# Kernel tuning notes

Measured on AMD Instinct MI355X. Metric: run time of the kernel, lower is better.

Reference implementation:

```python
import jax, jax.numpy as jnp
import numpy as np

N = 40000   # nodes
E = 640000  # edges (before self-loops)
G = 64      # graphs
EPS = 1e-5


def _gat_conv(x, src, dst, W, a_src, a_dst, bias, n_nodes):
    """PyG GATConv, heads=1, leaky_relu slope 0.2, with self-loops already in src/dst."""
    h = x @ W.T                              # [N, out]
    s_score = h @ a_src                      # [N]
    d_score = h @ a_dst                      # [N]
    e = jax.nn.leaky_relu(s_score[src] + d_score[dst], 0.2)  # [E]
    m = jax.ops.segment_max(e, dst, num_segments=n_nodes)
    ex = jnp.exp(e - m[dst])
    z = jax.ops.segment_sum(ex, dst, num_segments=n_nodes)
    alpha = ex / z[dst]                      # per-dst softmax over incoming edges
    out = jax.ops.segment_sum(h[src] * alpha[:, None], dst, num_segments=n_nodes)
    return out + bias


def _layer_norm(x, gamma, beta):
    mu = jnp.mean(x, axis=-1, keepdims=True)
    var = jnp.mean((x - mu) ** 2, axis=-1, keepdims=True)
    return gamma * (x - mu) * jax.lax.rsqrt(var + EPS) + beta


def setup_inputs() -> dict:
    key = jax.random.key(0)
    ks = jax.random.split(key, 16)
    x = jax.random.normal(ks[0], (N, 128), dtype=jnp.float32)
    edge_index = jax.random.randint(ks[1], (2, E), 0, N, dtype=jnp.int32)
    batch = jnp.sort(jax.random.randint(ks[2], (N,), 0, G, dtype=jnp.int32))
    def glorot(k, shape):
        fan = shape[-1]
        return jax.random.normal(k, shape, dtype=jnp.float32) / jnp.sqrt(jnp.float32(fan))
    return {
        "x": x, "edge_index": edge_index, "batch": batch,
        "W1": glorot(ks[3], (128, 128)), "a1_src": glorot(ks[4], (128,)),
        "a1_dst": glorot(ks[5], (128,)), "b1": jnp.zeros((128,), jnp.float32),
        "g1": jnp.ones((128,), jnp.float32), "be1": jnp.zeros((128,), jnp.float32),
        "W2": glorot(ks[6], (64, 128)), "a2_src": glorot(ks[7], (64,)),
        "a2_dst": glorot(ks[8], (64,)), "b2": jnp.zeros((64,), jnp.float32),
        "g2": jnp.ones((64,), jnp.float32), "be2": jnp.zeros((64,), jnp.float32),
        "Wl": glorot(ks[9], (64, 64)), "bl": jnp.zeros((64,), jnp.float32),
        "Wc": glorot(ks[10], (1, 64)), "bc": jnp.zeros((1,), jnp.float32),
    }


def reference(x, edge_index, batch, W1, a1_src, a1_dst, b1, g1, be1,
              W2, a2_src, a2_dst, b2, g2, be2, Wl, bl, Wc, bc):
    # add self-loops as PyG GATConv does by default
    loops = jnp.arange(N, dtype=edge_index.dtype)
    src = jnp.concatenate([edge_index[0], loops])
    dst = jnp.concatenate([edge_index[1], loops])

    h = jax.nn.relu(_gat_conv(x, src, dst, W1, a1_src, a1_dst, b1, N))
    h = _layer_norm(h, g1, be1)
    h = jax.nn.relu(_gat_conv(h, src, dst, W2, a2_src, a2_dst, b2, N))
    h = _layer_norm(h, g2, be2)

    # global mean pool over graphs
    sums = jax.ops.segment_sum(h, batch, num_segments=G)          # [G, 64]
    cnt = jax.ops.segment_sum(jnp.ones((N,), h.dtype), batch, num_segments=G)
    pooled = sums / jnp.maximum(cnt, 1.0)[:, None]

    out = pooled @ Wl.T + bl
    out = out @ Wc.T + bc                                          # [G, 1]
    return out.squeeze(-1)                                         # [G]
```

## Files before the change

kernel.cpp:

```cpp
#include <hip/hip_runtime.h>
#include <hip/hip_fp16.h>
#include <math.h>

#define NNODES 40000
#define NEDGES 640000
#define NGRAPH 64
#define CAP 96
constexpr float LN_EPS = 1e-5f;


__device__ __forceinline__ float bf_sum(float v) {
    #pragma unroll
    for (int o = 32; o > 0; o >>= 1) v += __shfl_xor(v, o);
    return v;
}

__global__ void prep(const float* __restrict__ W1, const float* __restrict__ W2,
                     float* __restrict__ Wt1, float* __restrict__ Wt2,
                     int* __restrict__ cnt, float* __restrict__ sums) {
    int t = blockIdx.x * 256 + threadIdx.x;
    if (t < NNODES) cnt[t] = 0;
    if (t < 128 * 128) { int o = t / 128, i = t % 128; Wt1[i * 128 + o] = W1[t]; }
    if (t < 64 * 128)  { int o = t / 128, i = t % 128; Wt2[i * 64 + o] = W2[t]; }
    if (t < NGRAPH * 64) sums[t] = 0.f;
}

__global__ void bin_edges(const int* __restrict__ ei, int E,
                          int* __restrict__ cnt, unsigned short* __restrict__ ssrc) {
    int e = blockIdx.x * blockDim.x + threadIdx.x;
    if (e >= E) return;
    int s = ei[e], d = ei[E + e];
    int pos = atomicAdd(cnt + d, 1);
    if (pos < CAP) ssrc[d * CAP + pos] = (unsigned short)s;
}

template<int DIN, int DOUT, int NPT>
__global__ __launch_bounds__(256) void gemm_scores(
        const float* __restrict__ X, const float* __restrict__ Wt,
        const float* __restrict__ asrc, const float* __restrict__ adst,
        __half* __restrict__ H, float* __restrict__ S, float* __restrict__ Dv) {
    constexpr int CHG = DOUT / 4;
    constexpr int NG  = 256 / CHG;
    constexpr int NPB = NG * NPT;
    static_assert(NPB == 64, "NPB must be 64");
    __shared__ float xs[DIN][NPB];
    __shared__ float ps[NG][NPT][2];
    const int base = blockIdx.x * NPB;
    const int tid = threadIdx.x;
    #pragma unroll
    for (int i4 = tid; i4 < NPB * DIN / 4; i4 += 256) {
        const int nd = i4 % NPB, c4 = i4 / NPB;
        float4 v = *(const float4*)(X + (size_t)(base + nd) * DIN + 4 * c4);
        xs[4 * c4 + 0][nd] = v.x;
        xs[4 * c4 + 1][nd] = v.y;
        xs[4 * c4 + 2][nd] = v.z;
        xs[4 * c4 + 3][nd] = v.w;
    }
    __syncthreads();
    const int cg = tid % CHG, ng = tid / CHG;
    const int c0 = 4 * cg, n0 = ng * NPT;
    float acc[NPT][4];
    #pragma unroll
    for (int n = 0; n < NPT; ++n)
        #pragma unroll
        for (int k = 0; k < 4; ++k) acc[n][k] = 0.f;
    #pragma unroll 2
    for (int i = 0; i < DIN; ++i) {
        const float4 w = *(const float4*)(Wt + i * DOUT + c0);
        #pragma unroll
        for (int n4 = 0; n4 < NPT / 4; ++n4) {
            const float4 xv = *(const float4*)&xs[i][n0 + 4 * n4];
            const float xf[4] = {xv.x, xv.y, xv.z, xv.w};
            #pragma unroll
            for (int j = 0; j < 4; ++j) {
                const int n = 4 * n4 + j;
                acc[n][0] += xf[j] * w.x; acc[n][1] += xf[j] * w.y;
                acc[n][2] += xf[j] * w.z; acc[n][3] += xf[j] * w.w;
            }
        }
    }
    #pragma unroll
    for (int n = 0; n < NPT; ++n) {
        __half2 p01 = __floats2half2_rn(acc[n][0], acc[n][1]);
        __half2 p23 = __floats2half2_rn(acc[n][2], acc[n][3]);
        __half2* hp = (__half2*)(H + (size_t)(base + n0 + n) * DOUT + c0);
        hp[0] = p01; hp[1] = p23;
    }
    const float4 asf = *(const float4*)(asrc + c0);
    const float4 adf = *(const float4*)(adst + c0);
    float sp[NPT], dp[NPT];
    #pragma unroll
    for (int n = 0; n < NPT; ++n) {
        sp[n] = acc[n][0]*asf.x + acc[n][1]*asf.y + acc[n][2]*asf.z + acc[n][3]*asf.w;
        dp[n] = acc[n][0]*adf.x + acc[n][1]*adf.y + acc[n][2]*adf.z + acc[n][3]*adf.w;
    }
    #pragma unroll
    for (int o = CHG / 2; o > 0; o >>= 1) {
        #pragma unroll
        for (int n = 0; n < NPT; ++n) {
            sp[n] += __shfl_xor(sp[n], o);
            dp[n] += __shfl_xor(dp[n], o);
        }
    }
    if (cg == 0) {
        #pragma unroll
        for (int n = 0; n < NPT; ++n) { ps[ng][n][0] = sp[n]; ps[ng][n][1] = dp[n]; }
    }
    __syncthreads();
    if (tid < NPB) {
        S[base + tid]  = ps[tid / NPT][tid % NPT][0];
        Dv[base + tid] = ps[tid / NPT][tid % NPT][1];
    }
}

template<int D>
__device__ __forceinline__ void aggr_one_generic(
        const int node, const int deg, const int lane,
        const unsigned short* __restrict__ ssrc, const float* __restrict__ S,
        const float dsc, const __half* __restrict__ H,
        float& acc0, float& acc1, float& z) {
    constexpr int VPL = D / 64;
    float zz = 0.f;
    const int r0 = node * CAP;
    for (int bse = 0; bse < deg; bse += 64) {
        const int n = min(64, deg - bse);
        int s = 0; float a = 0.f;
        if (lane < n) {
            s = ssrc[r0 + bse + lane];
            float t = S[s] + dsc;
            t = t > 0.f ? t : 0.2f * t;
            a = __expf(t);
        }
        zz += bf_sum(a);
        const int abits = __float_as_int(a);
        for (int j = 0; j < n; ++j) {
            const int sj = __builtin_amdgcn_readlane(s, j);
            const float aj = __int_as_float(__builtin_amdgcn_readlane(abits, j));
            const __half* hp = H + (size_t)sj * D;
            if (VPL == 1) {
                acc0 += aj * __half2float(hp[lane]);
            } else {
                const float2 f = __half22float2(*(const __half2*)(hp + 2 * lane));
                acc0 += aj * f.x; acc1 += aj * f.y;
            }
        }
    }
    z = zz;
}

template<int D, int POOL>
__device__ __forceinline__ void finish_node(
        const int node, const int lane,
        float acc0, float acc1, float z, const float aself, const float2 selfF,
        const float* __restrict__ b, const float* __restrict__ gam,
        const float* __restrict__ bet,
        float* __restrict__ out, const int* __restrict__ batch,
        float* __restrict__ sums) {
    constexpr int VPL = D / 64;
    acc0 += aself * selfF.x;
    if (VPL == 2) acc1 += aself * selfF.y;
    z += aself;
    const float zinv = 1.0f / z;
    float vv[VPL], lsum = 0.f;
    vv[0] = acc0;
    if (VPL == 2) vv[1] = acc1;
    #pragma unroll
    for (int k = 0; k < VPL; ++k) {
        const int ch = VPL * lane + k;
        vv[k] = fmaxf(vv[k] * zinv + b[ch], 0.f);
        lsum += vv[k];
    }
    const float mu = bf_sum(lsum) / D;
    float q = 0.f;
    #pragma unroll
    for (int k = 0; k < VPL; ++k) { vv[k] -= mu; q += vv[k] * vv[k]; }
    const float rstd = rsqrtf(bf_sum(q) / D + LN_EPS);
    #pragma unroll
    for (int k = 0; k < VPL; ++k) {
        const int ch = VPL * lane + k;
        vv[k] = gam[ch] * vv[k] * rstd + bet[ch];
    }
    if (POOL) {
        const int bg = batch[node];
        atomicAdd(&sums[bg * D + lane], vv[0]);
    } else {
        if (VPL == 1) out[(size_t)node * D + lane] = vv[0];
        else *(float2*)(out + (size_t)node * D + 2 * lane) = make_float2(vv[0], vv[1]);
    }
}

template<int D, int POOL>
__global__ __launch_bounds__(256) void gat_aggr(
        const int* __restrict__ cnt, const unsigned short* __restrict__ ssrc,
        const float* __restrict__ S, const float* __restrict__ Dv,
        const __half* __restrict__ H,
        const float* __restrict__ b, const float* __restrict__ gam,
        const float* __restrict__ bet,
        float* __restrict__ out, const int* __restrict__ batch,
        float* __restrict__ sums) {
    constexpr int VPL = D / 64;
    const int lane = threadIdx.x & 63;
    const int wv   = threadIdx.x >> 6;
    const int nodeA = blockIdx.x * 8 + wv * 2;
    const int nodeB = nodeA + 1;

    const int degA = min(__builtin_amdgcn_readfirstlane(cnt[nodeA]), CAP);
    const int degB = min(__builtin_amdgcn_readfirstlane(cnt[nodeB]), CAP);
    const float dscA = Dv[nodeA], dscB = Dv[nodeB];

    float tsA = S[nodeA] + dscA; tsA = tsA > 0.f ? tsA : 0.2f * tsA;
    float tsB = S[nodeB] + dscB; tsB = tsB > 0.f ? tsB : 0.2f * tsB;
    const float aselfA = __expf(tsA);
    const float aselfB = __expf(tsB);

    float2 selfFA, selfFB;
    if (VPL == 1) {
        selfFA = make_float2(__half2float(H[(size_t)nodeA * D + lane]), 0.f);
        selfFB = make_float2(__half2float(H[(size_t)nodeB * D + lane]), 0.f);
    } else {
        selfFA = __half22float2(*(const __half2*)(H + (size_t)nodeA * D + 2 * lane));
        selfFB = __half22float2(*(const __half2*)(H + (size_t)nodeB * D + 2 * lane));
    }

    float accA0 = 0.f, accA1 = 0.f, accB0 = 0.f, accB1 = 0.f;
    float zA, zB;

    if (degA <= 64 && degB <= 64) {
        int sA = 0, sB = 0;
        if (lane < degA) sA = ssrc[nodeA * CAP + lane];
        if (lane < degB) sB = ssrc[nodeB * CAP + lane];
        float tA = S[sA] + dscA;
        float tB = S[sB] + dscB;
        tA = tA > 0.f ? tA : 0.2f * tA;
        tB = tB > 0.f ? tB : 0.2f * tB;
        const float aA = (lane < degA) ? __expf(tA) : 0.f;
        const float aB = (lane < degB) ? __expf(tB) : 0.f;
        zA = bf_sum(aA);
        zB = bf_sum(aB);
        const int abA = __float_as_int(aA), abB = __float_as_int(aB);

        const int nmA = (degA + 7) & ~7;
        const int nmB = (degB + 7) & ~7;
        const int nmax = max(nmA, nmB);
        for (int j = 0; j < nmax; j += 8) {
            const bool doA = j < nmA, doB = j < nmB;
            float afA[8], afB[8];
            __half2 hvA[8], hvB[8];
            __half hsA[8], hsB[8];
            if (doA) {
                #pragma unroll
                for (int u = 0; u < 8; ++u) {
                    const int sj = __builtin_amdgcn_readlane(sA, j + u);
                    afA[u] = __int_as_float(__builtin_amdgcn_readlane(abA, j + u));
                    const __half* hp = H + (size_t)sj * D;
                    if (VPL == 1) hsA[u] = hp[lane];
                    else          hvA[u] = *(const __half2*)(hp + 2 * lane);
                }
            }
            if (doB) {
                #pragma unroll
                for (int u = 0; u < 8; ++u) {
                    const int sj = __builtin_amdgcn_readlane(sB, j + u);
                    afB[u] = __int_as_float(__builtin_amdgcn_readlane(abB, j + u));
                    const __half* hp = H + (size_t)sj * D;
                    if (VPL == 1) hsB[u] = hp[lane];
                    else          hvB[u] = *(const __half2*)(hp + 2 * lane);
                }
            }
            if (doA) {
                #pragma unroll
                for (int u = 0; u < 8; ++u) {
                    if (VPL == 1) {
                        accA0 += afA[u] * __half2float(hsA[u]);
                    } else {
                        accA0 += afA[u] * __half2float(__low2half(hvA[u]));
                        accA1 += afA[u] * __half2float(__high2half(hvA[u]));
                    }
                }
            }
            if (doB) {
                #pragma unroll
                for (int u = 0; u < 8; ++u) {
                    if (VPL == 1) {
                        accB0 += afB[u] * __half2float(hsB[u]);
                    } else {
                        accB0 += afB[u] * __half2float(__low2half(hvB[u]));
                        accB1 += afB[u] * __half2float(__high2half(hvB[u]));
                    }
                }
            }
        }
    } else {
        aggr_one_generic<D>(nodeA, degA, lane, ssrc, S, dscA, H, accA0, accA1, zA);
        aggr_one_generic<D>(nodeB, degB, lane, ssrc, S, dscB, H, accB0, accB1, zB);
    }

    finish_node<D, POOL>(nodeA, lane, accA0, accA1, zA, aselfA, selfFA,
                         b, gam, bet, out, batch, sums);
    finish_node<D, POOL>(nodeB, lane, accB0, accB1, zB, aselfB, selfFB,
                         b, gam, bet, out, batch, sums);
}

__global__ void final_head(const float* __restrict__ sums, const int* __restrict__ batch,
                           const float* __restrict__ Wl, const float* __restrict__ bl,
                           const float* __restrict__ Wc, const float* __restrict__ bc,
                           float* __restrict__ out) {
    __shared__ float p[64];
    __shared__ float red[64];
    const int g = blockIdx.x, tid = threadIdx.x;
    int lo = 0, hi = NNODES;
    while (lo < hi) { int mid = (lo + hi) >> 1; if (batch[mid] < g) lo = mid + 1; else hi = mid; }
    int lo2 = lo, hi2 = NNODES;
    while (lo2 < hi2) { int mid = (lo2 + hi2) >> 1; if (batch[mid] < g + 1) lo2 = mid + 1; else hi2 = mid; }
    const float cnt = (float)(lo2 - lo);
    p[tid] = sums[g * 64 + tid] / fmaxf(cnt, 1.0f);
    __syncthreads();
    float t = bl[tid];
    #pragma unroll 8
    for (int k = 0; k < 64; ++k) t += Wl[tid * 64 + k] * p[k];
    red[tid] = Wc[tid] * t;
    __syncthreads();
    for (int s = 32; s > 0; s >>= 1) {
        if (tid < s) red[tid] += red[tid + s];
        __syncthreads();
    }
    if (tid == 0) out[g] = red[0] + bc[0];
}

extern "C" void kernel_launch(void* const* d_in, const int* in_sizes, int n_in,
                              void* d_out, int out_size, void* d_ws, size_t ws_size,
                              hipStream_t stream) {
    const int N = NNODES, E = NEDGES, G = NGRAPH;

    const float* x      = (const float*)d_in[0];
    const int*   ei     = (const int*)d_in[1];
    const int*   batch  = (const int*)d_in[2];
    const float* W1     = (const float*)d_in[3];
    const float* a1s    = (const float*)d_in[4];
    const float* a1d    = (const float*)d_in[5];
    const float* b1     = (const float*)d_in[6];
    const float* g1     = (const float*)d_in[7];
    const float* be1    = (const float*)d_in[8];
    const float* W2     = (const float*)d_in[9];
    const float* a2s    = (const float*)d_in[10];
    const float* a2d    = (const float*)d_in[11];
    const float* b2     = (const float*)d_in[12];
    const float* g2     = (const float*)d_in[13];
    const float* be2    = (const float*)d_in[14];
    const float* Wl     = (const float*)d_in[15];
    const float* bl     = (const float*)d_in[16];
    const float* Wc     = (const float*)d_in[17];
    const float* bc     = (const float*)d_in[18];

    char* w = (char*)d_ws;
    __half* h1  = (__half*)w; w += (size_t)N * 128 * 2;
    float* acc1 = (float*)w; w += (size_t)N * 128 * 4;
    float* S    = (float*)w; w += (size_t)N * 4;
    float* Dv   = (float*)w; w += (size_t)N * 4;
    int* cnt    = (int*)w;   w += (size_t)N * 4;
    unsigned short* ssrc = (unsigned short*)w; w += (size_t)N * CAP * 2;
    float* Wt1  = (float*)w; w += (size_t)128 * 128 * 4;
    float* Wt2  = (float*)w; w += (size_t)128 * 64 * 4;
    float* sums = (float*)w; w += (size_t)G * 64 * 4;
    __half* h2 = h1;

    const int TB = 256;
    const int gridN = (N + 255) / 256;

    prep<<<gridN, 256, 0, stream>>>(W1, W2, Wt1, Wt2, cnt, sums);

    bin_edges<<<(E + TB - 1) / TB, TB, 0, stream>>>(ei, E, cnt, ssrc);

    gemm_scores<128, 128, 8><<<N / 64, 256, 0, stream>>>(x, Wt1, a1s, a1d, h1, S, Dv);
    gat_aggr<128, 0><<<N / 8, 256, 0, stream>>>(cnt, ssrc, S, Dv, h1, b1, g1, be1,
                                                acc1, nullptr, nullptr);

    gemm_scores<128, 64, 4><<<N / 64, 256, 0, stream>>>(acc1, Wt2, a2s, a2d, h2, S, Dv);
    gat_aggr<64, 1><<<N / 8, 256, 0, stream>>>(cnt, ssrc, S, Dv, h2, b2, g2, be2,
                                               nullptr, batch, sums);

    final_head<<<G, 64, 0, stream>>>(sums, batch, Wl, bl, Wc, bc, (float*)d_out);
}
```

Baseline: 270.6 us.

## Replace FP32 scalar GEMM with FP16 MFMA 16x16x32 in linear-score kernels

Both node-linear kernels now use the matrix cores via mfma_f32_16x16x32_f16. The weights are pre-packed in prep into per-lane fragment layout as fp16, and each wave loads its 16 input rows directly from global memory into registers, converting them to fp16. This drops the shared-memory staging and the scalar FMA loop. The attention score dot products are reduced with lane shuffles. Rounding inputs and weights to fp16 before the matmul adds precision error, and the per-element half stores to H are less coalesced than before.

```diff
diff --git a/kernel.cpp b/kernel.cpp
--- a/kernel.cpp
+++ b/kernel.cpp
@@ -9,6 +9,9 @@
 constexpr float LN_EPS = 1e-5f;
 
 
+typedef _Float16 v8h __attribute__((ext_vector_type(8)));
+typedef float    v4f __attribute__((ext_vector_type(4)));
+
 __device__ __forceinline__ float bf_sum(float v) {
     #pragma unroll
     for (int o = 32; o > 0; o >>= 1) v += __shfl_xor(v, o);
@@ -16,12 +19,22 @@
 }
 
 __global__ void prep(const float* __restrict__ W1, const float* __restrict__ W2,
-                     float* __restrict__ Wt1, float* __restrict__ Wt2,
+                     _Float16* __restrict__ Bf1, _Float16* __restrict__ Bf2,
                      int* __restrict__ cnt, float* __restrict__ sums) {
     int t = blockIdx.x * 256 + threadIdx.x;
     if (t < NNODES) cnt[t] = 0;
-    if (t < 128 * 128) { int o = t / 128, i = t % 128; Wt1[i * 128 + o] = W1[t]; }
-    if (t < 64 * 128)  { int o = t / 128, i = t % 128; Wt2[i * 64 + o] = W2[t]; }
+    if (t < 128 * 128) {
+        const int o = t >> 7, k = t & 127;
+        const int nt = o >> 4, lc = o & 15;
+        const int ks = k >> 5, g = (k >> 3) & 3, j = k & 7;
+        Bf1[(size_t)(((nt * 4 + ks) * 64 + g * 16 + lc) * 8 + j)] = (_Float16)W1[t];
+    }
+    if (t < 64 * 128) {
+        const int o = t >> 7, k = t & 127;
+        const int nt = o >> 4, lc = o & 15;
+        const int ks = k >> 5, g = (k >> 3) & 3, j = k & 7;
+        Bf2[(size_t)(((nt * 4 + ks) * 64 + g * 16 + lc) * 8 + j)] = (_Float16)W2[t];
+    }
     if (t < NGRAPH * 64) sums[t] = 0.f;
 }
 
@@ -34,82 +47,71 @@
     if (pos < CAP) ssrc[d * CAP + pos] = (unsigned short)s;
 }
 
-template<int DIN, int DOUT, int NPT>
-__global__ __launch_bounds__(256) void gemm_scores(
-        const float* __restrict__ X, const float* __restrict__ Wt,
+template<int DOUT>
+__global__ __launch_bounds__(256) void gemm_scores_mfma(
+        const float* __restrict__ X, const _Float16* __restrict__ Bfrag,
         const float* __restrict__ asrc, const float* __restrict__ adst,
         __half* __restrict__ H, float* __restrict__ S, float* __restrict__ Dv) {
-    constexpr int CHG = DOUT / 4;
-    constexpr int NG  = 256 / CHG;
-    constexpr int NPB = NG * NPT;
-    static_assert(NPB == 64, "NPB must be 64");
-    __shared__ float xs[DIN][NPB];
-    __shared__ float ps[NG][NPT][2];
-    const int base = blockIdx.x * NPB;
-    const int tid = threadIdx.x;
-    #pragma unroll
-    for (int i4 = tid; i4 < NPB * DIN / 4; i4 += 256) {
-        const int nd = i4 % NPB, c4 = i4 / NPB;
-        float4 v = *(const float4*)(X + (size_t)(base + nd) * DIN + 4 * c4);
-        xs[4 * c4 + 0][nd] = v.x;
-        xs[4 * c4 + 1][nd] = v.y;
-        xs[4 * c4 + 2][nd] = v.z;
-        xs[4 * c4 + 3][nd] = v.w;
-    }
-    __syncthreads();
-    const int cg = tid % CHG, ng = tid / CHG;
-    const int c0 = 4 * cg, n0 = ng * NPT;
-    float acc[NPT][4];
-    #pragma unroll
-    for (int n = 0; n < NPT; ++n)
+    constexpr int NT = DOUT / 16;
+    const int lane = threadIdx.x & 63;
+    const int wv   = threadIdx.x >> 6;
+    const int nb   = blockIdx.x * 64 + wv * 16;
+    const int lc = lane & 15, g = lane >> 4;
+
+    v8h a[4];
+    const float* xr = X + (size_t)(nb + lc) * 128 + g * 8;
+    #pragma unroll
+    for (int ks = 0; ks < 4; ++ks) {
+        const float4 lo = *(const float4*)(xr + ks * 32);
+        const float4 hi = *(const float4*)(xr + ks * 32 + 4);
+        v8h av;
+        av[0] = (_Float16)lo.x; av[1] = (_Float16)lo.y;
+        av[2] = (_Float16)lo.z; av[3] = (_Float16)lo.w;
+        av[4] = (_Float16)hi.x; av[5] = (_Float16)hi.y;
+        av[6] = (_Float16)hi.z; av[7] = (_Float16)hi.w;
+        a[ks] = av;
+    }
+
+    v4f acc[NT];
+    #pragma unroll
+    for (int nt = 0; nt < NT; ++nt) acc[nt] = (v4f){0.f, 0.f, 0.f, 0.f};
+
+    #pragma unroll
+    for (int ks = 0; ks < 4; ++ks) {
         #pragma unroll
-        for (int k = 0; k < 4; ++k) acc[n][k] = 0.f;
-    #pragma unroll 2
-    for (int i = 0; i < DIN; ++i) {
-        const float4 w = *(const float4*)(Wt + i * DOUT + c0);
+        for (int nt = 0; nt < NT; ++nt) {
+            const v8h bv = *(const v8h*)(Bfrag + (size_t)(((nt * 4 + ks) * 64 + lane) * 8));
+            acc[nt] = __builtin_amdgcn_mfma_f32_16x16x32_f16(a[ks], bv, acc[nt], 0, 0, 0);
+        }
+    }
+
+    float sp[4] = {0.f, 0.f, 0.f, 0.f}, dp[4] = {0.f, 0.f, 0.f, 0.f};
+    #pragma unroll
+    for (int nt = 0; nt < NT; ++nt) {
+        const float as_ = asrc[nt * 16 + lc];
+        const float ad_ = adst[nt * 16 + lc];
         #pragma unroll
-        for (int n4 = 0; n4 < NPT / 4; ++n4) {
-            const float4 xv = *(const float4*)&xs[i][n0 + 4 * n4];
-            const float xf[4] = {xv.x, xv.y, xv.z, xv.w};
-            #pragma unroll
-            for (int j = 0; j < 4; ++j) {
-                const int n = 4 * n4 + j;
-                acc[n][0] += xf[j] * w.x; acc[n][1] += xf[j] * w.y;
-                acc[n][2] += xf[j] * w.z; acc[n][3] += xf[j] * w.w;
-            }
-        }
-    }
-    #pragma unroll
-    for (int n = 0; n < NPT; ++n) {
-        __half2 p01 = __floats2half2_rn(acc[n][0], acc[n][1]);
-        __half2 p23 = __floats2half2_rn(acc[n][2], acc[n][3]);
-        __half2* hp = (__half2*)(H + (size_t)(base + n0 + n) * DOUT + c0);
-        hp[0] = p01; hp[1] = p23;
-    }
-    const float4 asf = *(const float4*)(asrc + c0);
-    const float4 adf = *(const float4*)(adst + c0);
-    float sp[NPT], dp[NPT];
-    #pragma unroll
-    for (int n = 0; n < NPT; ++n) {
-        sp[n] = acc[n][0]*asf.x + acc[n][1]*asf.y + acc[n][2]*asf.z + acc[n][3]*asf.w;
-        dp[n] = acc[n][0]*adf.x + acc[n][1]*adf.y + acc[n][2]*adf.z + acc[n][3]*adf.w;
-    }
-    #pragma unroll
-    for (int o = CHG / 2; o > 0; o >>= 1) {
+        for (int r = 0; r < 4; ++r) {
+            const float hv = acc[nt][r];
+            H[(size_t)(nb + g * 4 + r) * DOUT + nt * 16 + lc] = __float2half_rn(hv);
+            sp[r] += hv * as_;
+            dp[r] += hv * ad_;
+        }
+    }
+    #pragma unroll
+    for (int o = 8; o > 0; o >>= 1) {
         #pragma unroll
-        for (int n = 0; n < NPT; ++n) {
-            sp[n] += __shfl_xor(sp[n], o);
-            dp[n] += __shfl_xor(dp[n], o);
-        }
-    }
-    if (cg == 0) {
-        #pragma unroll
-        for (int n = 0; n < NPT; ++n) { ps[ng][n][0] = sp[n]; ps[ng][n][1] = dp[n]; }
-    }
-    __syncthreads();
-    if (tid < NPB) {
-        S[base + tid]  = ps[tid / NPT][tid % NPT][0];
-        Dv[base + tid] = ps[tid / NPT][tid % NPT][1];
+        for (int r = 0; r < 4; ++r) {
+            sp[r] += __shfl_xor(sp[r], o);
+            dp[r] += __shfl_xor(dp[r], o);
+        }
+    }
+    #pragma unroll
+    for (int r = 0; r < 4; ++r) {
+        if (lc == r) {
+            S[nb + g * 4 + r]  = sp[r];
+            Dv[nb + g * 4 + r] = dp[r];
+        }
     }
 }
 
@@ -359,23 +361,23 @@
     float* Dv   = (float*)w; w += (size_t)N * 4;
     int* cnt    = (int*)w;   w += (size_t)N * 4;
     unsigned short* ssrc = (unsigned short*)w; w += (size_t)N * CAP * 2;
-    float* Wt1  = (float*)w; w += (size_t)128 * 128 * 4;
-    float* Wt2  = (float*)w; w += (size_t)128 * 64 * 4;
+    _Float16* Bf1 = (_Float16*)w; w += (size_t)128 * 128 * 2;
+    _Float16* Bf2 = (_Float16*)w; w += (size_t)64 * 128 * 2;
     float* sums = (float*)w; w += (size_t)G * 64 * 4;
     __half* h2 = h1;
 
     const int TB = 256;
     const int gridN = (N + 255) / 256;
 
-    prep<<<gridN, 256, 0, stream>>>(W1, W2, Wt1, Wt2, cnt, sums);
+    prep<<<gridN, 256, 0, stream>>>(W1, W2, Bf1, Bf2, cnt, sums);
 
     bin_edges<<<(E + TB - 1) / TB, TB, 0, stream>>>(ei, E, cnt, ssrc);
 
-    gemm_scores<128, 128, 8><<<N / 64, 256, 0, stream>>>(x, Wt1, a1s, a1d, h1, S, Dv);
+    gemm_scores_mfma<128><<<N / 64, 256, 0, stream>>>(x, Bf1, a1s, a1d, h1, S, Dv);
     gat_aggr<128, 0><<<N / 8, 256, 0, stream>>>(cnt, ssrc, S, Dv, h1, b1, g1, be1,
                                                 acc1, nullptr, nullptr);
 
-    gemm_scores<128, 64, 4><<<N / 64, 256, 0, stream>>>(acc1, Wt2, a2s, a2d, h2, S, Dv);
+    gemm_scores_mfma<64><<<N / 64, 256, 0, stream>>>(acc1, Bf2, a2s, a2d, h2, S, Dv);
     gat_aggr<64, 1><<<N / 8, 256, 0, stream>>>(cnt, ssrc, S, Dv, h2, b2, g2, be2,
                                                nullptr, batch, sums);
 
```

After: 245.6 us. 1.1x faster.
